# Optimization experiments

Measured on AMD Instinct MI355X. Metric: run time of the kernel, lower is better.

## Reference

```python
import jax, jax.numpy as jnp
import numpy as np

EMBED_DIM = 2048
NUM_HEADS = 32
NUM_KV_HEADS = 8
HEAD_DIM = EMBED_DIM // NUM_HEADS  # 64
GROUPS = NUM_HEADS // NUM_KV_HEADS  # 4
BSZ, SEQ = 1, 2048


def apply_rope(x, cos, sin):
    # x: [b, s, h, d]; cos/sin: [s, d//2]. Interleaved-pair (view_as_complex) convention.
    x1 = x[..., 0::2]
    x2 = x[..., 1::2]
    c = cos[None, :, None, :]
    s = sin[None, :, None, :]
    o1 = x1 * c - x2 * s
    o2 = x1 * s + x2 * c
    return jnp.stack([o1, o2], axis=-1).reshape(x.shape)


def setup_inputs() -> dict:
    key = jax.random.key(0)
    ks = jax.random.split(key, 10)
    sc = 1.0 / np.sqrt(EMBED_DIM)
    return {
        "query_states": jax.random.normal(ks[0], (BSZ, SEQ, EMBED_DIM), jnp.float32),
        "key_value_states": jax.random.normal(ks[1], (BSZ, SEQ, EMBED_DIM), jnp.float32),
        "cos_q": jax.random.uniform(ks[2], (SEQ, HEAD_DIM // 2), jnp.float32),
        "sin_q": jax.random.uniform(ks[3], (SEQ, HEAD_DIM // 2), jnp.float32),
        "cos_k": jax.random.uniform(ks[4], (SEQ, HEAD_DIM // 2), jnp.float32),
        "sin_k": jax.random.uniform(ks[5], (SEQ, HEAD_DIM // 2), jnp.float32),
        "attention_mask": jnp.ones((BSZ, SEQ), dtype=bool),
        "wq": jax.random.normal(ks[6], (EMBED_DIM, EMBED_DIM), jnp.float32) * sc,
        "wk": jax.random.normal(ks[7], (NUM_KV_HEADS * HEAD_DIM, EMBED_DIM), jnp.float32) * sc,
        "wv": jax.random.normal(ks[8], (NUM_KV_HEADS * HEAD_DIM, EMBED_DIM), jnp.float32) * sc,
        "wo": jax.random.normal(ks[9], (EMBED_DIM, EMBED_DIM), jnp.float32) * sc,
    }


def reference(query_states, key_value_states, cos_q, sin_q, cos_k, sin_k,
              attention_mask, wq, wk, wv, wo):
    b, ql, _ = query_states.shape
    _, kl, _ = key_value_states.shape
    # Projections (torch Linear, no bias: x @ W.T)
    q = jnp.einsum('bsd,od->bso', query_states, wq).reshape(b, ql, NUM_HEADS, HEAD_DIM)
    k = jnp.einsum('bsd,od->bso', key_value_states, wk).reshape(b, kl, NUM_KV_HEADS, HEAD_DIM)
    v = jnp.einsum('bsd,od->bso', key_value_states, wv).reshape(b, kl, NUM_KV_HEADS, HEAD_DIM)
    q = apply_rope(q, cos_q, sin_q)
    k = apply_rope(k, cos_k, sin_k)
    # GQA without materializing expanded K/V: q heads grouped as (g, kv_head)
    # torch's unsqueeze(2).expand.reshape maps head h -> kv head h % NUM_KV_HEADS,
    # with group index g = h // NUM_KV_HEADS.
    qg = q.transpose(0, 2, 1, 3).reshape(b, GROUPS, NUM_KV_HEADS, ql, HEAD_DIM)
    kt = k.transpose(0, 2, 1, 3)  # [b, kvh, kl, d]
    vt = v.transpose(0, 2, 1, 3)
    scale = 1.0 / jnp.sqrt(jnp.asarray(HEAD_DIM, q.dtype))
    scores = jnp.einsum('bgkqd,bksd->bgkqs', qg, kt) * scale  # [b,g,kvh,ql,kl]
    neg = jnp.asarray(jnp.finfo(scores.dtype).min, scores.dtype)
    scores = jnp.where(attention_mask[:, None, None, None, :], scores, neg)
    probs = jax.nn.softmax(scores, axis=-1)
    out = jnp.einsum('bgkqs,bksd->bgkqd', probs, vt)  # [b,g,kvh,ql,d]
    out = out.reshape(b, NUM_HEADS, ql, HEAD_DIM).transpose(0, 2, 1, 3).reshape(b, ql, NUM_HEADS * HEAD_DIM)
    return jnp.einsum('bso,do->bsd', out, wo)
```

## Files before the change

kernel.cpp:

```cpp
#include <hip/hip_runtime.h>
#include <cstdint>

#define SEQ 2048
#define ED  2048
#define NHEADS 32
#define NKV 8
#define HD 64
#define KVD 512

typedef __attribute__((ext_vector_type(8))) short short8;
typedef __attribute__((ext_vector_type(8))) unsigned short ushort8;
typedef __attribute__((ext_vector_type(4))) float f32x4;

__device__ __forceinline__ float bf2f(unsigned short u){ return __uint_as_float(((unsigned)u)<<16); }
__device__ __forceinline__ unsigned short f2bf(float f){
  unsigned x = __float_as_uint(f);
  return (unsigned short)((x + 0x7fffu + ((x>>16)&1u)) >> 16);
}

__device__ __forceinline__ void gld_lds16(const void* g, void* l){
  __builtin_amdgcn_global_load_lds((const __attribute__((address_space(1))) unsigned*)g,
                                   (__attribute__((address_space(3))) unsigned*)l, 16, 0, 0);
}

__global__ __launch_bounds__(256) void cvt_all(const float* __restrict__ Xq, const float* __restrict__ Xkv,
                                               const float* __restrict__ wq, const float* __restrict__ wk,
                                               const float* __restrict__ wv, const float* __restrict__ wo,
                                               unsigned short* __restrict__ Xb, unsigned short* __restrict__ KVb,
                                               unsigned short* __restrict__ Wqb, unsigned short* __restrict__ WKVb,
                                               unsigned short* __restrict__ Wob){
  int b = blockIdx.x;
  const float* src; unsigned short* dst;
  if (b < 2048)      { src = Xq;  dst = Xb; }
  else if (b < 4096) { src = Xkv; dst = KVb;  b -= 2048; }
  else if (b < 6144) { src = wq;  dst = Wqb;  b -= 4096; }
  else if (b < 6656) { src = wk;  dst = WKVb; b -= 6144; }
  else if (b < 7168) { src = wv;  dst = WKVb + (size_t)512*ED; b -= 6656; }
  else               { src = wo;  dst = Wob;  b -= 7168; }
  size_t t = (size_t)b*256 + threadIdx.x;
  const f32x4* p = (const f32x4*)src + t*2;
  f32x4 a = p[0], c = p[1];
  ushort8 o;
  o[0]=f2bf(a[0]); o[1]=f2bf(a[1]); o[2]=f2bf(a[2]); o[3]=f2bf(a[3]);
  o[4]=f2bf(c[0]); o[5]=f2bf(c[1]); o[6]=f2bf(c[2]); o[7]=f2bf(c[3]);
  *(ushort8*)(dst + t*8) = o;
}

__global__ __launch_bounds__(256) void rope_all(unsigned short* __restrict__ Qb, unsigned short* __restrict__ Kbuf,
                                                const float* __restrict__ cq, const float* __restrict__ sq,
                                                const float* __restrict__ ck, const float* __restrict__ sk){
  int b = blockIdx.x;
  unsigned short* buf; const float* cosT; const float* sinT; int lw; float scale;
  if (b < 2048){ buf=Qb; cosT=cq; sinT=sq; lw=11; scale=0.125f*1.44269504088896f; }
  else { b -= 2048; buf=Kbuf; cosT=ck; sinT=sk; lw=9; scale=1.0f; }
  int t = b*256 + threadIdx.x;
  int e = t*8;
  int s = e >> lw;
  int col = e & ((1<<lw)-1);
  int i0 = (col & 63) >> 1;
  ushort8 v = *(ushort8*)(buf + e);
  f32x4 c  = *(const f32x4*)(cosT + s*32 + i0);
  f32x4 sn = *(const f32x4*)(sinT + s*32 + i0);
  ushort8 o;
#pragma unroll
  for(int p=0;p<4;p++){
    float x1 = bf2f(v[2*p]), x2 = bf2f(v[2*p+1]);
    o[2*p]   = f2bf((x1*c[p] - x2*sn[p])*scale);
    o[2*p+1] = f2bf((x1*sn[p] + x2*c[p])*scale);
  }
  *(ushort8*)(buf + e) = o;
}

template<int EPI>
__device__ __forceinline__ void gemm_body(const unsigned short* __restrict__ A,
                                          const unsigned short* __restrict__ B,
                                          void* __restrict__ Cout, void* __restrict__ Cout2,
                                          int M, int N, int K, int bx, int by,
                                          unsigned short* As, unsigned short* Bs){
  const int tid = threadIdx.x;
  const int lane = tid & 63;
  const int wave = tid >> 6;
  const int wr = wave >> 1, wc = wave & 1;
  const int m0 = by * 128, n0 = bx * 128;
  const int l15 = lane & 15, l4 = lane >> 4;

  f32x4 acc[4][4] = {};

  const int arow0 = tid>>2,        sc0 = tid&3, oc0 = sc0 ^ (arow0 & 3);
  const int arow1 = (tid+256)>>2,  oc1 = sc0 ^ (arow1 & 3);
  const unsigned short* Ag0 = A + (size_t)(m0+arow0)*K + oc0*8;
  const unsigned short* Ag1 = A + (size_t)(m0+arow1)*K + oc1*8;
  const unsigned short* Bg0 = B + (size_t)(n0+arow0)*K + oc0*8;
  const unsigned short* Bg1 = B + (size_t)(n0+arow1)*K + oc1*8;

  const int nk = K >> 5;
  gld_lds16(Ag0, As + tid*8);
  gld_lds16(Ag1, As + (tid+256)*8);
  gld_lds16(Bg0, Bs + tid*8);
  gld_lds16(Bg1, Bs + (tid+256)*8);
  __syncthreads();

  for(int kt=0; kt<nk; kt++){
    const int cur = (kt&1)*4096;
    if (kt+1 < nk){
      const int nxt = cur ^ 4096;
      const int ko = (kt+1)*32;
      gld_lds16(Ag0 + ko, As + nxt + tid*8);
      gld_lds16(Ag1 + ko, As + nxt + (tid+256)*8);
      gld_lds16(Bg0 + ko, Bs + nxt + tid*8);
      gld_lds16(Bg1 + ko, Bs + nxt + (tid+256)*8);
    }
    short8 af[4], bfr[4];
#pragma unroll
    for(int m=0;m<4;m++){
      int row = wr*64 + m*16 + l15;
      af[m] = *(const short8*)&As[cur + row*32 + ((l4 ^ (row&3))*8)];
    }
#pragma unroll
    for(int n=0;n<4;n++){
      int row = wc*64 + n*16 + l15;
      bfr[n] = *(const short8*)&Bs[cur + row*32 + ((l4 ^ (row&3))*8)];
    }
#pragma unroll
    for(int m=0;m<4;m++)
#pragma unroll
      for(int n=0;n<4;n++)
        acc[m][n] = __builtin_amdgcn_mfma_f32_16x16x32_bf16(af[m], bfr[n], acc[m][n], 0,0,0);
    __syncthreads();
  }

#pragma unroll
  for(int m=0;m<4;m++){
    const int row0 = m0 + wr*64 + m*16 + l4*4;
#pragma unroll
    for(int n=0;n<4;n++){
      const int col = n0 + wc*64 + n*16 + l15;
      if constexpr (EPI == 0){
        unsigned short* C = (unsigned short*)Cout;
#pragma unroll
        for(int r=0;r<4;r++) C[(size_t)(row0+r)*N + col] = f2bf(acc[m][n][r]);
      } else if constexpr (EPI == 2){
        float* C = (float*)Cout;
#pragma unroll
        for(int r=0;r<4;r++) C[(size_t)(row0+r)*N + col] = acc[m][n][r];
      } else {
        if (n0 < 512){
          unsigned short* C = (unsigned short*)Cout;
#pragma unroll
          for(int r=0;r<4;r++) C[(size_t)(row0+r)*512 + col] = f2bf(acc[m][n][r]);
        } else {
          unsigned short* C = (unsigned short*)Cout2;
          const int d = col - 512;
#pragma unroll
          for(int r=0;r<4;r++){
            int seq = row0 + r;
            int pos = ((seq>>5)&1)*32 + (seq&15)*2 + ((seq>>4)&1);
            C[(size_t)d*SEQ + (seq & ~63) + pos] = f2bf(acc[m][n][r]);
          }
        }
      }
    }
  }
}

__global__ __launch_bounds__(256) void gemm_proj(const unsigned short* __restrict__ Xb,
                                                 const unsigned short* __restrict__ Wqb,
                                                 const unsigned short* __restrict__ KVb,
                                                 const unsigned short* __restrict__ WKVb,
                                                 unsigned short* __restrict__ Qb,
                                                 unsigned short* __restrict__ Kb,
                                                 unsigned short* __restrict__ Vtb){
  __shared__ unsigned short As[2*128*32];
  __shared__ unsigned short Bs[2*128*32];
  int b = blockIdx.x;
  if (b < 256){
    gemm_body<0>(Xb, Wqb, Qb, nullptr, SEQ, ED, ED, b&15, b>>4, As, Bs);
  } else {
    int bb = b - 256;
    gemm_body<3>(KVb, WKVb, Kb, Vtb, SEQ, 1024, ED, bb&7, bb>>3, As, Bs);
  }
}

__global__ __launch_bounds__(256) void gemm_out_k(const unsigned short* __restrict__ Obf,
                                                  const unsigned short* __restrict__ Wob,
                                                  float* __restrict__ out){
  __shared__ unsigned short As[2*128*32];
  __shared__ unsigned short Bs[2*128*32];
  int b = blockIdx.x;
  gemm_body<2>(Obf, Wob, out, nullptr, SEQ, ED, ED, b&15, b>>4, As, Bs);
}

__global__ __launch_bounds__(256) void attn_k(const unsigned short* __restrict__ Qb,
                                              const unsigned short* __restrict__ Kb,
                                              const unsigned short* __restrict__ Vt,
                                              unsigned short* __restrict__ Ob){
  __shared__ unsigned short Ks[2][64*64];
  __shared__ unsigned short Vs[2][64*64];
  __shared__ unsigned Psu[4][512];
  const int tid = threadIdx.x, lane = tid & 63, w = tid >> 6;
  const int l15 = lane & 15, l4 = lane >> 4;
  const int qb = blockIdx.x, h = blockIdx.y, kvh = h & 7;

  const int row = tid>>3, sc = tid&7, oc = sc ^ (row&7);
  const int row2 = row + 32, oc2 = sc ^ (row2&7);
  const unsigned short* Kg0 = Kb + (size_t)row*KVD  + kvh*HD + oc*8;
  const unsigned short* Kg1 = Kb + (size_t)row2*KVD + kvh*HD + oc2*8;
  const unsigned short* Vg0 = Vt + (size_t)(kvh*HD+row)*SEQ  + oc*8;
  const unsigned short* Vg1 = Vt + (size_t)(kvh*HD+row2)*SEQ + oc2*8;

#define ATTN_STAGE(buf, kb_) { \
    const size_t koff = (size_t)(kb_)*64*KVD; const int voff = (kb_)*64; \
    gld_lds16(Kg0 + koff, &Ks[buf][tid*8]); \
    gld_lds16(Kg1 + koff, &Ks[buf][(tid+256)*8]); \
    gld_lds16(Vg0 + voff, &Vs[buf][tid*8]); \
    gld_lds16(Vg1 + voff, &Vs[buf][(tid+256)*8]); }

  ATTN_STAGE(0, 0);

  short8 qa[2];
  {
    const unsigned short* qp = Qb + (size_t)(qb*64 + w*16 + l15)*ED + h*HD + l4*8;
    qa[0] = *(const short8*)qp;
    qa[1] = *(const short8*)(qp + 32);
  }

  unsigned* Pw = &Psu[w][0];
  int pwi[4][2];
#pragma unroll
  for(int r=0;r<4;r++){
    int q = l4*4 + r;
#pragma unroll
    for(int ks=0;ks<2;ks++){
      int chunk = ks*4 + (l15>>2);
      pwi[r][ks] = q*32 + ((chunk ^ (q&7))<<2) + (l15&3);
    }
  }
  const int rdi0 = l15*32 + ((l4       ^ (l15&7))<<2);
  const int rdi1 = l15*32 + (((4+l4)   ^ (l15&7))<<2);

  f32x4 o_acc[4] = {};
  float l_acc[4] = {0.f,0.f,0.f,0.f};
  __syncthreads();

  for(int kb=0; kb<SEQ/64; kb++){
    const int cur = kb & 1;
    if (kb+1 < SEQ/64) ATTN_STAGE(cur^1, kb+1);

    __builtin_amdgcn_s_setprio(1);
    f32x4 s_acc[4] = {};
#pragma unroll
    for(int n=0;n<4;n++){
      int key = n*16 + l15;
#pragma unroll
      for(int ks=0;ks<2;ks++){
        short8 kf = *(const short8*)&Ks[cur][key*64 + (((ks*4+l4) ^ (key&7))*8)];
        s_acc[n] = __builtin_amdgcn_mfma_f32_16x16x32_bf16(qa[ks], kf, s_acc[n], 0,0,0);
      }
    }
    __builtin_amdgcn_s_setprio(0);

#pragma unroll
    for(int r=0;r<4;r++){
      float p0 = exp2f(s_acc[0][r]), p1 = exp2f(s_acc[1][r]);
      float p2 = exp2f(s_acc[2][r]), p3 = exp2f(s_acc[3][r]);
      l_acc[r] += (p0+p1)+(p2+p3);
      unsigned u01, u23;
      asm("v_cvt_pk_bf16_f32 %0, %1, %2" : "=v"(u01) : "v"(p0), "v"(p1));
      asm("v_cvt_pk_bf16_f32 %0, %1, %2" : "=v"(u23) : "v"(p2), "v"(p3));
      Pw[pwi[r][0]] = u01;
      Pw[pwi[r][1]] = u23;
    }
    asm volatile("s_waitcnt lgkmcnt(0)" ::: "memory");

    __builtin_amdgcn_s_setprio(1);
#pragma unroll
    for(int ks=0;ks<2;ks++){
      short8 pa = *(const short8*)&Pw[ks ? rdi1 : rdi0];
#pragma unroll
      for(int n=0;n<4;n++){
        int d = n*16 + l15;
        short8 vf = *(const short8*)&Vs[cur][d*64 + (((ks*4+l4) ^ (d&7))*8)];
        o_acc[n] = __builtin_amdgcn_mfma_f32_16x16x32_bf16(pa, vf, o_acc[n], 0,0,0);
      }
    }
    __builtin_amdgcn_s_setprio(0);
    __syncthreads();
  }
#undef ATTN_STAGE

#pragma unroll
  for(int r=0;r<4;r++){
    float t = l_acc[r];
    t += __shfl_xor(t,1); t += __shfl_xor(t,2); t += __shfl_xor(t,4); t += __shfl_xor(t,8);
    l_acc[r] = 1.0f / t;
  }
#pragma unroll
  for(int n=0;n<4;n++){
    const int col = h*HD + n*16 + l15;
#pragma unroll
    for(int r=0;r<4;r++){
      const int srow = qb*64 + w*16 + l4*4 + r;
      Ob[(size_t)srow*ED + col] = f2bf(o_acc[n][r] * l_acc[r]);
    }
  }
}

extern "C" void kernel_launch(void* const* d_in, const int* in_sizes, int n_in,
                              void* d_out, int out_size, void* d_ws, size_t ws_size,
                              hipStream_t stream) {
  const float* Xq    = (const float*)d_in[0];
  const float* Xkv   = (const float*)d_in[1];
  const float* cos_q = (const float*)d_in[2];
  const float* sin_q = (const float*)d_in[3];
  const float* cos_k = (const float*)d_in[4];
  const float* sin_k = (const float*)d_in[5];
  const float* wq = (const float*)d_in[7];
  const float* wk = (const float*)d_in[8];
  const float* wv = (const float*)d_in[9];
  const float* wo = (const float*)d_in[10];
  float* out = (float*)d_out;

  char* ws = (char*)d_ws;
  const size_t MB = 1u<<20;
  unsigned short* Xb   = (unsigned short*)(ws + 0*MB);
  unsigned short* KVb  = (unsigned short*)(ws + 8*MB);
  unsigned short* Wqb  = (unsigned short*)(ws + 16*MB);
  unsigned short* WKVb = (unsigned short*)(ws + 24*MB);
  unsigned short* Wob  = (unsigned short*)(ws + 28*MB);
  unsigned short* Qb   = (unsigned short*)(ws + 36*MB);
  unsigned short* Kb   = (unsigned short*)(ws + 44*MB);
  unsigned short* Vtb  = (unsigned short*)(ws + 46*MB);
  unsigned short* Obf  = (unsigned short*)(ws + 48*MB);

  cvt_all<<<9216,256,0,stream>>>(Xq, Xkv, wq, wk, wv, wo, Xb, KVb, Wqb, WKVb, Wob);

  gemm_proj<<<384,256,0,stream>>>(Xb, Wqb, KVb, WKVb, Qb, Kb, Vtb);

  rope_all<<<2560,256,0,stream>>>(Qb, Kb, cos_q, sin_q, cos_k, sin_k);

  attn_k<<<dim3(SEQ/64, NHEADS),256,0,stream>>>(Qb, Kb, Vtb, Obf);

  gemm_out_k<<<256,256,0,stream>>>(Obf, Wob, out);
}
```

Before: 308.8 us.

## Split-K GEMMs with atomic fp32 accumulation and double query tile per wave in attention

The projection and output GEMMs now split K in two, accumulate into fp32 buffers with atomic adds, and zero those buffers with memsets beforehand. The rope kernel reads the fp32 projections and converts Q, K and Vt to bf16 itself. The attention kernel processes 32 query rows per wave (128 per block), which halves the grid and reuses each K/V LDS tile across two MFMA row tiles. The aim is more blocks for the small GEMM grids on many CUs and less K/V reload traffic in attention. The cost is atomic traffic, extra memsets, larger fp32 intermediates and non-deterministic summation order.

```diff
diff --git a/kernel.cpp b/kernel.cpp
--- a/kernel.cpp
+++ b/kernel.cpp
@@ -46,36 +46,51 @@
   *(ushort8*)(dst + t*8) = o;
 }
 
-__global__ __launch_bounds__(256) void rope_all(unsigned short* __restrict__ Qb, unsigned short* __restrict__ Kbuf,
+__global__ __launch_bounds__(256) void rope_cvt(const float* __restrict__ Qf, const float* __restrict__ Kf,
+                                                const float* __restrict__ Vtf,
+                                                unsigned short* __restrict__ Qb, unsigned short* __restrict__ Kb,
+                                                unsigned short* __restrict__ Vtb,
                                                 const float* __restrict__ cq, const float* __restrict__ sq,
                                                 const float* __restrict__ ck, const float* __restrict__ sk){
   int b = blockIdx.x;
-  unsigned short* buf; const float* cosT; const float* sinT; int lw; float scale;
-  if (b < 2048){ buf=Qb; cosT=cq; sinT=sq; lw=11; scale=0.125f*1.44269504088896f; }
-  else { b -= 2048; buf=Kbuf; cosT=ck; sinT=sk; lw=9; scale=1.0f; }
+  if (b >= 2560){
+    size_t t = (size_t)(b-2560)*256 + threadIdx.x;
+    const f32x4* p = (const f32x4*)Vtf + t*2;
+    f32x4 a = p[0], c = p[1];
+    ushort8 o;
+    o[0]=f2bf(a[0]); o[1]=f2bf(a[1]); o[2]=f2bf(a[2]); o[3]=f2bf(a[3]);
+    o[4]=f2bf(c[0]); o[5]=f2bf(c[1]); o[6]=f2bf(c[2]); o[7]=f2bf(c[3]);
+    *(ushort8*)(Vtb + t*8) = o;
+    return;
+  }
+  const float* src; unsigned short* dst; const float* cosT; const float* sinT; int lw; float scale;
+  if (b < 2048){ src=Qf; dst=Qb; cosT=cq; sinT=sq; lw=11; scale=0.125f*1.44269504088896f; }
+  else { b -= 2048; src=Kf; dst=Kb; cosT=ck; sinT=sk; lw=9; scale=1.0f; }
   int t = b*256 + threadIdx.x;
   int e = t*8;
   int s = e >> lw;
   int col = e & ((1<<lw)-1);
   int i0 = (col & 63) >> 1;
-  ushort8 v = *(ushort8*)(buf + e);
+  const f32x4* p = (const f32x4*)(src + e);
+  f32x4 x0 = p[0], x1 = p[1];
   f32x4 c  = *(const f32x4*)(cosT + s*32 + i0);
   f32x4 sn = *(const f32x4*)(sinT + s*32 + i0);
   ushort8 o;
-#pragma unroll
-  for(int p=0;p<4;p++){
-    float x1 = bf2f(v[2*p]), x2 = bf2f(v[2*p+1]);
-    o[2*p]   = f2bf((x1*c[p] - x2*sn[p])*scale);
-    o[2*p+1] = f2bf((x1*sn[p] + x2*c[p])*scale);
-  }
-  *(ushort8*)(buf + e) = o;
+  float xs[8] = {x0[0],x0[1],x0[2],x0[3],x1[0],x1[1],x1[2],x1[3]};
+#pragma unroll
+  for(int q=0;q<4;q++){
+    float a1 = xs[2*q], a2 = xs[2*q+1];
+    o[2*q]   = f2bf((a1*c[q] - a2*sn[q])*scale);
+    o[2*q+1] = f2bf((a1*sn[q] + a2*c[q])*scale);
+  }
+  *(ushort8*)(dst + e) = o;
 }
 
 template<int EPI>
 __device__ __forceinline__ void gemm_body(const unsigned short* __restrict__ A,
                                           const unsigned short* __restrict__ B,
-                                          void* __restrict__ Cout, void* __restrict__ Cout2,
-                                          int M, int N, int K, int bx, int by,
+                                          float* __restrict__ C, float* __restrict__ C2,
+                                          int M, int N, int K, int bx, int by, int ksplit,
                                           unsigned short* As, unsigned short* Bs){
   const int tid = threadIdx.x;
   const int lane = tid & 63;
@@ -83,17 +98,18 @@
   const int wr = wave >> 1, wc = wave & 1;
   const int m0 = by * 128, n0 = bx * 128;
   const int l15 = lane & 15, l4 = lane >> 4;
+  const int kbase = ksplit * (K >> 1);
 
   f32x4 acc[4][4] = {};
 
   const int arow0 = tid>>2,        sc0 = tid&3, oc0 = sc0 ^ (arow0 & 3);
   const int arow1 = (tid+256)>>2,  oc1 = sc0 ^ (arow1 & 3);
-  const unsigned short* Ag0 = A + (size_t)(m0+arow0)*K + oc0*8;
-  const unsigned short* Ag1 = A + (size_t)(m0+arow1)*K + oc1*8;
-  const unsigned short* Bg0 = B + (size_t)(n0+arow0)*K + oc0*8;
-  const unsigned short* Bg1 = B + (size_t)(n0+arow1)*K + oc1*8;
-
-  const int nk = K >> 5;
+  const unsigned short* Ag0 = A + (size_t)(m0+arow0)*K + kbase + oc0*8;
+  const unsigned short* Ag1 = A + (size_t)(m0+arow1)*K + kbase + oc1*8;
+  const unsigned short* Bg0 = B + (size_t)(n0+arow0)*K + kbase + oc0*8;
+  const unsigned short* Bg1 = B + (size_t)(n0+arow1)*K + kbase + oc1*8;
+
+  const int nk = K >> 6;
   gld_lds16(Ag0, As + tid*8);
   gld_lds16(Ag1, As + (tid+256)*8);
   gld_lds16(Bg0, Bs + tid*8);
@@ -135,27 +151,20 @@
 #pragma unroll
     for(int n=0;n<4;n++){
       const int col = n0 + wc*64 + n*16 + l15;
-      if constexpr (EPI == 0){
-        unsigned short* C = (unsigned short*)Cout;
-#pragma unroll
-        for(int r=0;r<4;r++) C[(size_t)(row0+r)*N + col] = f2bf(acc[m][n][r]);
-      } else if constexpr (EPI == 2){
-        float* C = (float*)Cout;
-#pragma unroll
-        for(int r=0;r<4;r++) C[(size_t)(row0+r)*N + col] = acc[m][n][r];
+      if constexpr (EPI == 10){
+#pragma unroll
+        for(int r=0;r<4;r++) unsafeAtomicAdd(&C[(size_t)(row0+r)*N + col], acc[m][n][r]);
       } else {
         if (n0 < 512){
-          unsigned short* C = (unsigned short*)Cout;
-#pragma unroll
-          for(int r=0;r<4;r++) C[(size_t)(row0+r)*512 + col] = f2bf(acc[m][n][r]);
+#pragma unroll
+          for(int r=0;r<4;r++) unsafeAtomicAdd(&C[(size_t)(row0+r)*512 + col], acc[m][n][r]);
         } else {
-          unsigned short* C = (unsigned short*)Cout2;
           const int d = col - 512;
 #pragma unroll
           for(int r=0;r<4;r++){
             int seq = row0 + r;
             int pos = ((seq>>5)&1)*32 + (seq&15)*2 + ((seq>>4)&1);
-            C[(size_t)d*SEQ + (seq & ~63) + pos] = f2bf(acc[m][n][r]);
+            unsafeAtomicAdd(&C2[(size_t)d*SEQ + (seq & ~63) + pos], acc[m][n][r]);
           }
         }
       }
@@ -167,17 +176,19 @@
                                                  const unsigned short* __restrict__ Wqb,
                                                  const unsigned short* __restrict__ KVb,
                                                  const unsigned short* __restrict__ WKVb,
-                                                 unsigned short* __restrict__ Qb,
-                                                 unsigned short* __restrict__ Kb,
-                                                 unsigned short* __restrict__ Vtb){
+                                                 float* __restrict__ Qf,
+                                                 float* __restrict__ Kf,
+                                                 float* __restrict__ Vtf){
   __shared__ unsigned short As[2*128*32];
   __shared__ unsigned short Bs[2*128*32];
   int b = blockIdx.x;
-  if (b < 256){
-    gemm_body<0>(Xb, Wqb, Qb, nullptr, SEQ, ED, ED, b&15, b>>4, As, Bs);
+  if (b < 512){
+    int s = b>>8, rem = b & 255;
+    gemm_body<10>(Xb, Wqb, Qf, nullptr, SEQ, ED, ED, rem&15, rem>>4, s, As, Bs);
   } else {
-    int bb = b - 256;
-    gemm_body<3>(KVb, WKVb, Kb, Vtb, SEQ, 1024, ED, bb&7, bb>>3, As, Bs);
+    int bb = b - 512;
+    int s = bb>>7, rem = bb & 127;
+    gemm_body<13>(KVb, WKVb, Kf, Vtf, SEQ, 1024, ED, rem&7, rem>>3, s, As, Bs);
   }
 }
 
@@ -187,16 +198,17 @@
   __shared__ unsigned short As[2*128*32];
   __shared__ unsigned short Bs[2*128*32];
   int b = blockIdx.x;
-  gemm_body<2>(Obf, Wob, out, nullptr, SEQ, ED, ED, b&15, b>>4, As, Bs);
+  int s = b>>8, rem = b & 255;
+  gemm_body<10>(Obf, Wob, out, nullptr, SEQ, ED, ED, rem&15, rem>>4, s, As, Bs);
 }
 
 __global__ __launch_bounds__(256) void attn_k(const unsigned short* __restrict__ Qb,
                                               const unsigned short* __restrict__ Kb,
                                               const unsigned short* __restrict__ Vt,
                                               unsigned short* __restrict__ Ob){
-  __shared__ unsigned short Ks[2][64*64];
-  __shared__ unsigned short Vs[2][64*64];
-  __shared__ unsigned Psu[4][512];
+  __shared__ unsigned short Ks[2][4096];
+  __shared__ unsigned short Vs[2][4096];
+  __shared__ unsigned Psu[4][1024];
   const int tid = threadIdx.x, lane = tid & 63, w = tid >> 6;
   const int l15 = lane & 15, l4 = lane >> 4;
   const int qb = blockIdx.x, h = blockIdx.y, kvh = h & 7;
@@ -217,29 +229,19 @@
 
   ATTN_STAGE(0, 0);
 
-  short8 qa[2];
+  short8 qa[2][2];
   {
-    const unsigned short* qp = Qb + (size_t)(qb*64 + w*16 + l15)*ED + h*HD + l4*8;
-    qa[0] = *(const short8*)qp;
-    qa[1] = *(const short8*)(qp + 32);
+    const unsigned short* qp0 = Qb + (size_t)(qb*128 + w*32 + l15)*ED + h*HD + l4*8;
+    qa[0][0] = *(const short8*)qp0;
+    qa[0][1] = *(const short8*)(qp0 + 32);
+    const unsigned short* qp1 = qp0 + (size_t)16*ED;
+    qa[1][0] = *(const short8*)qp1;
+    qa[1][1] = *(const short8*)(qp1 + 32);
   }
 
   unsigned* Pw = &Psu[w][0];
-  int pwi[4][2];
-#pragma unroll
-  for(int r=0;r<4;r++){
-    int q = l4*4 + r;
-#pragma unroll
-    for(int ks=0;ks<2;ks++){
-      int chunk = ks*4 + (l15>>2);
-      pwi[r][ks] = q*32 + ((chunk ^ (q&7))<<2) + (l15&3);
-    }
-  }
-  const int rdi0 = l15*32 + ((l4       ^ (l15&7))<<2);
-  const int rdi1 = l15*32 + (((4+l4)   ^ (l15&7))<<2);
-
-  f32x4 o_acc[4] = {};
-  float l_acc[4] = {0.f,0.f,0.f,0.f};
+  f32x4 o_acc[2][4] = {};
+  float l_acc[2][4] = {{0.f,0.f,0.f,0.f},{0.f,0.f,0.f,0.f}};
   __syncthreads();
 
   for(int kb=0; kb<SEQ/64; kb++){
@@ -247,40 +249,47 @@
     if (kb+1 < SEQ/64) ATTN_STAGE(cur^1, kb+1);
 
     __builtin_amdgcn_s_setprio(1);
-    f32x4 s_acc[4] = {};
+    f32x4 s_acc[2][4] = {};
 #pragma unroll
     for(int n=0;n<4;n++){
       int key = n*16 + l15;
 #pragma unroll
       for(int ks=0;ks<2;ks++){
         short8 kf = *(const short8*)&Ks[cur][key*64 + (((ks*4+l4) ^ (key&7))*8)];
-        s_acc[n] = __builtin_amdgcn_mfma_f32_16x16x32_bf16(qa[ks], kf, s_acc[n], 0,0,0);
+        s_acc[0][n] = __builtin_amdgcn_mfma_f32_16x16x32_bf16(qa[0][ks], kf, s_acc[0][n], 0,0,0);
+        s_acc[1][n] = __builtin_amdgcn_mfma_f32_16x16x32_bf16(qa[1][ks], kf, s_acc[1][n], 0,0,0);
       }
     }
     __builtin_amdgcn_s_setprio(0);
 
 #pragma unroll
-    for(int r=0;r<4;r++){
-      float p0 = exp2f(s_acc[0][r]), p1 = exp2f(s_acc[1][r]);
-      float p2 = exp2f(s_acc[2][r]), p3 = exp2f(s_acc[3][r]);
-      l_acc[r] += (p0+p1)+(p2+p3);
-      unsigned u01, u23;
-      asm("v_cvt_pk_bf16_f32 %0, %1, %2" : "=v"(u01) : "v"(p0), "v"(p1));
-      asm("v_cvt_pk_bf16_f32 %0, %1, %2" : "=v"(u23) : "v"(p2), "v"(p3));
-      Pw[pwi[r][0]] = u01;
-      Pw[pwi[r][1]] = u23;
+    for(int mt=0;mt<2;mt++){
+#pragma unroll
+      for(int r=0;r<4;r++){
+        float p0 = exp2f(s_acc[mt][0][r]), p1 = exp2f(s_acc[mt][1][r]);
+        float p2 = exp2f(s_acc[mt][2][r]), p3 = exp2f(s_acc[mt][3][r]);
+        l_acc[mt][r] += (p0+p1)+(p2+p3);
+        unsigned u01, u23;
+        asm("v_cvt_pk_bf16_f32 %0, %1, %2" : "=v"(u01) : "v"(p0), "v"(p1));
+        asm("v_cvt_pk_bf16_f32 %0, %1, %2" : "=v"(u23) : "v"(p2), "v"(p3));
+        const int q32 = mt*16 + l4*4 + r;
+        Pw[q32*32 + (((l15>>2)     ^ (q32&7))<<2) + (l15&3)] = u01;
+        Pw[q32*32 + (((4+(l15>>2)) ^ (q32&7))<<2) + (l15&3)] = u23;
+      }
     }
     asm volatile("s_waitcnt lgkmcnt(0)" ::: "memory");
 
     __builtin_amdgcn_s_setprio(1);
 #pragma unroll
     for(int ks=0;ks<2;ks++){
-      short8 pa = *(const short8*)&Pw[ks ? rdi1 : rdi0];
+      short8 pa0 = *(const short8*)&Pw[(l15     )*32 + (((ks*4+l4) ^ (l15&7))<<2)];
+      short8 pa1 = *(const short8*)&Pw[(16+l15  )*32 + (((ks*4+l4) ^ (l15&7))<<2)];
 #pragma unroll
       for(int n=0;n<4;n++){
         int d = n*16 + l15;
         short8 vf = *(const short8*)&Vs[cur][d*64 + (((ks*4+l4) ^ (d&7))*8)];
-        o_acc[n] = __builtin_amdgcn_mfma_f32_16x16x32_bf16(pa, vf, o_acc[n], 0,0,0);
+        o_acc[0][n] = __builtin_amdgcn_mfma_f32_16x16x32_bf16(pa0, vf, o_acc[0][n], 0,0,0);
+        o_acc[1][n] = __builtin_amdgcn_mfma_f32_16x16x32_bf16(pa1, vf, o_acc[1][n], 0,0,0);
       }
     }
     __builtin_amdgcn_s_setprio(0);
@@ -289,20 +298,24 @@
 #undef ATTN_STAGE
 
 #pragma unroll
-  for(int r=0;r<4;r++){
-    float t = l_acc[r];
-    t += __shfl_xor(t,1); t += __shfl_xor(t,2); t += __shfl_xor(t,4); t += __shfl_xor(t,8);
-    l_acc[r] = 1.0f / t;
-  }
-#pragma unroll
-  for(int n=0;n<4;n++){
-    const int col = h*HD + n*16 + l15;
+  for(int mt=0;mt<2;mt++)
 #pragma unroll
     for(int r=0;r<4;r++){
-      const int srow = qb*64 + w*16 + l4*4 + r;
-      Ob[(size_t)srow*ED + col] = f2bf(o_acc[n][r] * l_acc[r]);
-    }
-  }
+      float t = l_acc[mt][r];
+      t += __shfl_xor(t,1); t += __shfl_xor(t,2); t += __shfl_xor(t,4); t += __shfl_xor(t,8);
+      l_acc[mt][r] = 1.0f / t;
+    }
+#pragma unroll
+  for(int mt=0;mt<2;mt++)
+#pragma unroll
+    for(int n=0;n<4;n++){
+      const int col = h*HD + n*16 + l15;
+#pragma unroll
+      for(int r=0;r<4;r++){
+        const int srow = qb*128 + w*32 + mt*16 + l4*4 + r;
+        Ob[(size_t)srow*ED + col] = f2bf(o_acc[mt][n][r] * l_acc[mt][r]);
+      }
+    }
 }
 
 extern "C" void kernel_launch(void* const* d_in, const int* in_sizes, int n_in,
@@ -327,18 +340,24 @@
   unsigned short* Wqb  = (unsigned short*)(ws + 16*MB);
   unsigned short* WKVb = (unsigned short*)(ws + 24*MB);
   unsigned short* Wob  = (unsigned short*)(ws + 28*MB);
-  unsigned short* Qb   = (unsigned short*)(ws + 36*MB);
-  unsigned short* Kb   = (unsigned short*)(ws + 44*MB);
-  unsigned short* Vtb  = (unsigned short*)(ws + 46*MB);
-  unsigned short* Obf  = (unsigned short*)(ws + 48*MB);
+  float*          Qf   = (float*)(ws + 36*MB);
+  float*          Kf   = (float*)(ws + 52*MB);
+  float*          Vtf  = (float*)(ws + 56*MB);
+  unsigned short* Qb   = (unsigned short*)(ws + 60*MB);
+  unsigned short* Kb   = (unsigned short*)(ws + 68*MB);
+  unsigned short* Vtb  = (unsigned short*)(ws + 70*MB);
+  unsigned short* Obf  = (unsigned short*)(ws + 36*MB);
+
+  hipMemsetAsync(ws + 36*MB, 0, 24*MB, stream);
+  hipMemsetAsync(out, 0, (size_t)SEQ*ED*sizeof(float), stream);
 
   cvt_all<<<9216,256,0,stream>>>(Xq, Xkv, wq, wk, wv, wo, Xb, KVb, Wqb, WKVb, Wob);
 
-  gemm_proj<<<384,256,0,stream>>>(Xb, Wqb, KVb, WKVb, Qb, Kb, Vtb);
-
-  rope_all<<<2560,256,0,stream>>>(Qb, Kb, cos_q, sin_q, cos_k, sin_k);
-
-  attn_k<<<dim3(SEQ/64, NHEADS),256,0,stream>>>(Qb, Kb, Vtb, Obf);
-
-  gemm_out_k<<<256,256,0,stream>>>(Obf, Wob, out);
-}
+  gemm_proj<<<768,256,0,stream>>>(Xb, Wqb, KVb, WKVb, Qf, Kf, Vtf);
+
+  rope_cvt<<<3072,256,0,stream>>>(Qf, Kf, Vtf, Qb, Kb, Vtb, cos_q, sin_q, cos_k, sin_k);
+
+  attn_k<<<dim3(SEQ/128, NHEADS),256,0,stream>>>(Qb, Kb, Vtb, Obf);
+
+  gemm_out_k<<<512,256,0,stream>>>(Obf, Wob, out);
+}
```

Result: slower. 369.5 us (+19.7%).

## Triple-buffer GEMM loads with one barrier and double attention query tile per wave

Applied to the files above, without the earlier changes.

The GEMM main loop moves from double to triple buffering. It keeps two stages in flight, waits on vmcnt counts, and uses a single raw barrier per iteration instead of two syncthreads. The LDS swizzle changes to XOR on (row>>1) to cut bank conflicts, and the MFMA block gets raised priority. The attention kernel now has each wave process 32 query rows (two 16-row tiles), so every K/V fragment read from LDS is reused twice and the grid is halved, at the cost of more registers and fewer blocks.

```diff
diff --git a/kernel.cpp b/kernel.cpp
--- a/kernel.cpp
+++ b/kernel.cpp
@@ -86,48 +86,54 @@
 
   f32x4 acc[4][4] = {};
 
-  const int arow0 = tid>>2,        sc0 = tid&3, oc0 = sc0 ^ (arow0 & 3);
-  const int arow1 = (tid+256)>>2,  oc1 = sc0 ^ (arow1 & 3);
+  const int arow0 = tid>>2,        sc0 = tid&3, oc0 = sc0 ^ ((arow0>>1) & 3);
+  const int arow1 = (tid+256)>>2,  oc1 = sc0 ^ ((arow1>>1) & 3);
   const unsigned short* Ag0 = A + (size_t)(m0+arow0)*K + oc0*8;
   const unsigned short* Ag1 = A + (size_t)(m0+arow1)*K + oc1*8;
   const unsigned short* Bg0 = B + (size_t)(n0+arow0)*K + oc0*8;
   const unsigned short* Bg1 = B + (size_t)(n0+arow1)*K + oc1*8;
 
   const int nk = K >> 5;
-  gld_lds16(Ag0, As + tid*8);
-  gld_lds16(Ag1, As + (tid+256)*8);
-  gld_lds16(Bg0, Bs + tid*8);
-  gld_lds16(Bg1, Bs + (tid+256)*8);
-  __syncthreads();
+
+#define GSTAGE(buf_, kt_) { \
+    const int ko_ = (kt_)*32; const int bo_ = (buf_)*4096; \
+    gld_lds16(Ag0 + ko_, As + bo_ + tid*8); \
+    gld_lds16(Ag1 + ko_, As + bo_ + (tid+256)*8); \
+    gld_lds16(Bg0 + ko_, Bs + bo_ + tid*8); \
+    gld_lds16(Bg1 + ko_, Bs + bo_ + (tid+256)*8); }
+
+  GSTAGE(0, 0);
+  GSTAGE(1, 1);
 
   for(int kt=0; kt<nk; kt++){
-    const int cur = (kt&1)*4096;
-    if (kt+1 < nk){
-      const int nxt = cur ^ 4096;
-      const int ko = (kt+1)*32;
-      gld_lds16(Ag0 + ko, As + nxt + tid*8);
-      gld_lds16(Ag1 + ko, As + nxt + (tid+256)*8);
-      gld_lds16(Bg0 + ko, Bs + nxt + tid*8);
-      gld_lds16(Bg1 + ko, Bs + nxt + (tid+256)*8);
-    }
+    if (kt+1 == nk) { asm volatile("s_waitcnt vmcnt(0)" ::: "memory"); }
+    else            { asm volatile("s_waitcnt vmcnt(4)" ::: "memory"); }
+    __builtin_amdgcn_s_barrier();
+    __builtin_amdgcn_sched_barrier(0);
+
+    if (kt+2 < nk) GSTAGE((kt+2)%3, kt+2);
+
+    const int cur = (kt%3)*4096;
     short8 af[4], bfr[4];
 #pragma unroll
     for(int m=0;m<4;m++){
       int row = wr*64 + m*16 + l15;
-      af[m] = *(const short8*)&As[cur + row*32 + ((l4 ^ (row&3))*8)];
+      af[m] = *(const short8*)&As[cur + row*32 + ((l4 ^ ((row>>1)&3))*8)];
     }
 #pragma unroll
     for(int n=0;n<4;n++){
       int row = wc*64 + n*16 + l15;
-      bfr[n] = *(const short8*)&Bs[cur + row*32 + ((l4 ^ (row&3))*8)];
-    }
+      bfr[n] = *(const short8*)&Bs[cur + row*32 + ((l4 ^ ((row>>1)&3))*8)];
+    }
+    __builtin_amdgcn_s_setprio(1);
 #pragma unroll
     for(int m=0;m<4;m++)
 #pragma unroll
       for(int n=0;n<4;n++)
         acc[m][n] = __builtin_amdgcn_mfma_f32_16x16x32_bf16(af[m], bfr[n], acc[m][n], 0,0,0);
-    __syncthreads();
-  }
+    __builtin_amdgcn_s_setprio(0);
+  }
+#undef GSTAGE
 
 #pragma unroll
   for(int m=0;m<4;m++){
@@ -170,8 +176,8 @@
                                                  unsigned short* __restrict__ Qb,
                                                  unsigned short* __restrict__ Kb,
                                                  unsigned short* __restrict__ Vtb){
-  __shared__ unsigned short As[2*128*32];
-  __shared__ unsigned short Bs[2*128*32];
+  __shared__ unsigned short As[3*4096];
+  __shared__ unsigned short Bs[3*4096];
   int b = blockIdx.x;
   if (b < 256){
     gemm_body<0>(Xb, Wqb, Qb, nullptr, SEQ, ED, ED, b&15, b>>4, As, Bs);
@@ -184,8 +190,8 @@
 __global__ __launch_bounds__(256) void gemm_out_k(const unsigned short* __restrict__ Obf,
                                                   const unsigned short* __restrict__ Wob,
                                                   float* __restrict__ out){
-  __shared__ unsigned short As[2*128*32];
-  __shared__ unsigned short Bs[2*128*32];
+  __shared__ unsigned short As[3*4096];
+  __shared__ unsigned short Bs[3*4096];
   int b = blockIdx.x;
   gemm_body<2>(Obf, Wob, out, nullptr, SEQ, ED, ED, b&15, b>>4, As, Bs);
 }
@@ -194,9 +200,9 @@
                                               const unsigned short* __restrict__ Kb,
                                               const unsigned short* __restrict__ Vt,
                                               unsigned short* __restrict__ Ob){
-  __shared__ unsigned short Ks[2][64*64];
-  __shared__ unsigned short Vs[2][64*64];
-  __shared__ unsigned Psu[4][512];
+  __shared__ unsigned short Ks[2][4096];
+  __shared__ unsigned short Vs[2][4096];
+  __shared__ unsigned Psu[4][1024];
   const int tid = threadIdx.x, lane = tid & 63, w = tid >> 6;
   const int l15 = lane & 15, l4 = lane >> 4;
   const int qb = blockIdx.x, h = blockIdx.y, kvh = h & 7;
@@ -217,29 +223,19 @@
 
   ATTN_STAGE(0, 0);
 
-  short8 qa[2];
+  short8 qa[2][2];
   {
-    const unsigned short* qp = Qb + (size_t)(qb*64 + w*16 + l15)*ED + h*HD + l4*8;
-    qa[0] = *(const short8*)qp;
-    qa[1] = *(const short8*)(qp + 32);
+    const unsigned short* qp0 = Qb + (size_t)(qb*128 + w*32 + l15)*ED + h*HD + l4*8;
+    qa[0][0] = *(const short8*)qp0;
+    qa[0][1] = *(const short8*)(qp0 + 32);
+    const unsigned short* qp1 = qp0 + (size_t)16*ED;
+    qa[1][0] = *(const short8*)qp1;
+    qa[1][1] = *(const short8*)(qp1 + 32);
   }
 
   unsigned* Pw = &Psu[w][0];
-  int pwi[4][2];
-#pragma unroll
-  for(int r=0;r<4;r++){
-    int q = l4*4 + r;
-#pragma unroll
-    for(int ks=0;ks<2;ks++){
-      int chunk = ks*4 + (l15>>2);
-      pwi[r][ks] = q*32 + ((chunk ^ (q&7))<<2) + (l15&3);
-    }
-  }
-  const int rdi0 = l15*32 + ((l4       ^ (l15&7))<<2);
-  const int rdi1 = l15*32 + (((4+l4)   ^ (l15&7))<<2);
-
-  f32x4 o_acc[4] = {};
-  float l_acc[4] = {0.f,0.f,0.f,0.f};
+  f32x4 o_acc[2][4] = {};
+  float l_acc[2][4] = {{0.f,0.f,0.f,0.f},{0.f,0.f,0.f,0.f}};
   __syncthreads();
 
   for(int kb=0; kb<SEQ/64; kb++){
@@ -247,40 +243,47 @@
     if (kb+1 < SEQ/64) ATTN_STAGE(cur^1, kb+1);
 
     __builtin_amdgcn_s_setprio(1);
-    f32x4 s_acc[4] = {};
+    f32x4 s_acc[2][4] = {};
 #pragma unroll
     for(int n=0;n<4;n++){
       int key = n*16 + l15;
 #pragma unroll
       for(int ks=0;ks<2;ks++){
         short8 kf = *(const short8*)&Ks[cur][key*64 + (((ks*4+l4) ^ (key&7))*8)];
-        s_acc[n] = __builtin_amdgcn_mfma_f32_16x16x32_bf16(qa[ks], kf, s_acc[n], 0,0,0);
+        s_acc[0][n] = __builtin_amdgcn_mfma_f32_16x16x32_bf16(qa[0][ks], kf, s_acc[0][n], 0,0,0);
+        s_acc[1][n] = __builtin_amdgcn_mfma_f32_16x16x32_bf16(qa[1][ks], kf, s_acc[1][n], 0,0,0);
       }
     }
     __builtin_amdgcn_s_setprio(0);
 
 #pragma unroll
-    for(int r=0;r<4;r++){
-      float p0 = exp2f(s_acc[0][r]), p1 = exp2f(s_acc[1][r]);
-      float p2 = exp2f(s_acc[2][r]), p3 = exp2f(s_acc[3][r]);
-      l_acc[r] += (p0+p1)+(p2+p3);
-      unsigned u01, u23;
-      asm("v_cvt_pk_bf16_f32 %0, %1, %2" : "=v"(u01) : "v"(p0), "v"(p1));
-      asm("v_cvt_pk_bf16_f32 %0, %1, %2" : "=v"(u23) : "v"(p2), "v"(p3));
-      Pw[pwi[r][0]] = u01;
-      Pw[pwi[r][1]] = u23;
+    for(int mt=0;mt<2;mt++){
+#pragma unroll
+      for(int r=0;r<4;r++){
+        float p0 = exp2f(s_acc[mt][0][r]), p1 = exp2f(s_acc[mt][1][r]);
+        float p2 = exp2f(s_acc[mt][2][r]), p3 = exp2f(s_acc[mt][3][r]);
+        l_acc[mt][r] += (p0+p1)+(p2+p3);
+        unsigned u01, u23;
+        asm("v_cvt_pk_bf16_f32 %0, %1, %2" : "=v"(u01) : "v"(p0), "v"(p1));
+        asm("v_cvt_pk_bf16_f32 %0, %1, %2" : "=v"(u23) : "v"(p2), "v"(p3));
+        const int q32 = mt*16 + l4*4 + r;
+        Pw[q32*32 + (((l15>>2)     ^ (q32&7))<<2) + (l15&3)] = u01;
+        Pw[q32*32 + (((4+(l15>>2)) ^ (q32&7))<<2) + (l15&3)] = u23;
+      }
     }
     asm volatile("s_waitcnt lgkmcnt(0)" ::: "memory");
 
     __builtin_amdgcn_s_setprio(1);
 #pragma unroll
     for(int ks=0;ks<2;ks++){
-      short8 pa = *(const short8*)&Pw[ks ? rdi1 : rdi0];
+      short8 pa0 = *(const short8*)&Pw[(l15     )*32 + (((ks*4+l4) ^ (l15&7))<<2)];
+      short8 pa1 = *(const short8*)&Pw[(16+l15  )*32 + (((ks*4+l4) ^ (l15&7))<<2)];
 #pragma unroll
       for(int n=0;n<4;n++){
         int d = n*16 + l15;
         short8 vf = *(const short8*)&Vs[cur][d*64 + (((ks*4+l4) ^ (d&7))*8)];
-        o_acc[n] = __builtin_amdgcn_mfma_f32_16x16x32_bf16(pa, vf, o_acc[n], 0,0,0);
+        o_acc[0][n] = __builtin_amdgcn_mfma_f32_16x16x32_bf16(pa0, vf, o_acc[0][n], 0,0,0);
+        o_acc[1][n] = __builtin_amdgcn_mfma_f32_16x16x32_bf16(pa1, vf, o_acc[1][n], 0,0,0);
       }
     }
     __builtin_amdgcn_s_setprio(0);
@@ -289,20 +292,24 @@
 #undef ATTN_STAGE
 
 #pragma unroll
-  for(int r=0;r<4;r++){
-    float t = l_acc[r];
-    t += __shfl_xor(t,1); t += __shfl_xor(t,2); t += __shfl_xor(t,4); t += __shfl_xor(t,8);
-    l_acc[r] = 1.0f / t;
-  }
-#pragma unroll
-  for(int n=0;n<4;n++){
-    const int col = h*HD + n*16 + l15;
+  for(int mt=0;mt<2;mt++)
 #pragma unroll
     for(int r=0;r<4;r++){
-      const int srow = qb*64 + w*16 + l4*4 + r;
-      Ob[(size_t)srow*ED + col] = f2bf(o_acc[n][r] * l_acc[r]);
-    }
-  }
+      float t = l_acc[mt][r];
+      t += __shfl_xor(t,1); t += __shfl_xor(t,2); t += __shfl_xor(t,4); t += __shfl_xor(t,8);
+      l_acc[mt][r] = 1.0f / t;
+    }
+#pragma unroll
+  for(int mt=0;mt<2;mt++)
+#pragma unroll
+    for(int n=0;n<4;n++){
+      const int col = h*HD + n*16 + l15;
+#pragma unroll
+      for(int r=0;r<4;r++){
+        const int srow = qb*128 + w*32 + mt*16 + l4*4 + r;
+        Ob[(size_t)srow*ED + col] = f2bf(o_acc[mt][n][r] * l_acc[mt][r]);
+      }
+    }
 }
 
 extern "C" void kernel_launch(void* const* d_in, const int* in_sizes, int n_in,
@@ -338,7 +345,7 @@
 
   rope_all<<<2560,256,0,stream>>>(Qb, Kb, cos_q, sin_q, cos_k, sin_k);
 
-  attn_k<<<dim3(SEQ/64, NHEADS),256,0,stream>>>(Qb, Kb, Vtb, Obf);
+  attn_k<<<dim3(SEQ/128, NHEADS),256,0,stream>>>(Qb, Kb, Vtb, Obf);
 
   gemm_out_k<<<256,256,0,stream>>>(Obf, Wob, out);
 }
```

Measured after the change: 283.7 us. -8.1%, faster.
